# Optimization experiments

Hardware: AMD Instinct MI355X
Metric: run time of the kernel (lower is better)

Reference implementation:

```python
import jax, jax.numpy as jnp
import numpy as np

D_MODEL = 2048
N_HEADS = 16
HEAD_DIM = D_MODEL // N_HEADS


def _rotate_half(x):
    # matches torch: x1 = x[..., ::2], x2 = x[..., 1::2]; cat(-x2, x1)
    x1 = x[..., ::2]
    x2 = x[..., 1::2]
    return jnp.concatenate((-x2, x1), axis=-1)


def _rope_sin_cos(seq_len, dtype):
    # NOTE: module builds RoPE tables over the FULL d_model, then truncates to head_dim.
    inv_freq = 1.0 / (10000.0 ** (np.arange(0, D_MODEL, 2, dtype=np.float32) / D_MODEL))
    pos = np.arange(seq_len, dtype=np.float32)
    freqs = pos[:, None] * inv_freq[None, :]          # [S, d_model/2]
    sin = jnp.asarray(np.sin(freqs)[:, :HEAD_DIM], dtype=dtype)  # [S, head_dim]
    cos = jnp.asarray(np.cos(freqs)[:, :HEAD_DIM], dtype=dtype)
    return sin[None, None], cos[None, None]           # [1,1,S,head_dim]


def setup_inputs() -> dict:
    key = jax.random.key(0)
    ks = jax.random.split(key, 11)
    B, S = 2, 2048
    sc = 1.0 / np.sqrt(D_MODEL)
    inp = {
        "query": jax.random.normal(ks[0], (B, S, D_MODEL), jnp.float32),
        "key": jax.random.normal(ks[1], (B, S, D_MODEL), jnp.float32),
        "value": jax.random.normal(ks[2], (B, S, D_MODEL), jnp.float32),
        "Wq": jax.random.normal(ks[3], (D_MODEL, D_MODEL), jnp.float32) * sc,
        "bq": jnp.zeros((D_MODEL,), jnp.float32),
        "Wk": jax.random.normal(ks[4], (D_MODEL, D_MODEL), jnp.float32) * sc,
        "bk": jnp.zeros((D_MODEL,), jnp.float32),
        "Wv": jax.random.normal(ks[5], (D_MODEL, D_MODEL), jnp.float32) * sc,
        "bv": jnp.zeros((D_MODEL,), jnp.float32),
        "Wo": jax.random.normal(ks[6], (D_MODEL, D_MODEL), jnp.float32) * sc,
        "bo": jnp.zeros((D_MODEL,), jnp.float32),
    }
    return inp


def reference(query, key, value, Wq, bq, Wk, bk, Wv, bv, Wo, bo):
    B, S, _ = query.shape

    def split_heads(x):
        return x.reshape(B, S, N_HEADS, HEAD_DIM).transpose(0, 2, 1, 3)  # [B,H,S,d_k]

    Q = split_heads(query @ Wq.T + bq)
    K = split_heads(key @ Wk.T + bk)
    V = split_heads(value @ Wv.T + bv)

    sin, cos = _rope_sin_cos(S, Q.dtype)
    Q = Q * cos + _rotate_half(Q) * sin
    K = K * cos + _rotate_half(K) * sin

    scores = jnp.einsum("bhqd,bhkd->bhqk", Q, K) / np.sqrt(HEAD_DIM)
    probs = jax.nn.softmax(scores, axis=-1)  # dropout is identity at eval
    context = jnp.einsum("bhqk,bhkd->bhqd", probs, V)
    out = context.transpose(0, 2, 1, 3).reshape(B, S, D_MODEL)
    return out @ Wo.T + bo
```

## Files before the change

kernel.cpp:

```cpp
#include <hip/hip_runtime.h>
#include <hip/hip_bf16.h>

#define D_MODEL 2048
#define SEQ     2048
#define BATCH   2
#define NH      16
#define HD      128
#define MROWS   (BATCH*SEQ)

typedef __attribute__((ext_vector_type(8)))  short bf16x8;
typedef __attribute__((ext_vector_type(4)))  float f32x4;
typedef __attribute__((ext_vector_type(16))) float f32x16;
typedef __attribute__((ext_vector_type(4)))  unsigned int u32x4;

static __device__ __forceinline__ void lds16(const void* g, void* l) {
    __builtin_amdgcn_global_load_lds(
        (const __attribute__((address_space(1))) void*)g,
        (__attribute__((address_space(3))) void*)l,
        16, 0, 0);
}

static __device__ __forceinline__ unsigned int pk2(float a, float b) {
    const unsigned int lo = __bfloat16_as_ushort(__float2bfloat16(a));
    const unsigned int hh = __bfloat16_as_ushort(__float2bfloat16(b));
    return lo | (hh << 16);
}
static __device__ __forceinline__ unsigned short bfu(float a) {
    return __bfloat16_as_ushort(__float2bfloat16(a));
}

__global__ __launch_bounds__(256) void cvt_all(
    const float* __restrict__ q,  const float* __restrict__ k,  const float* __restrict__ v,
    const float* __restrict__ wq, const float* __restrict__ wk, const float* __restrict__ wv,
    const float* __restrict__ wo,
    unsigned short* __restrict__ qb, unsigned short* __restrict__ kb, unsigned short* __restrict__ vb,
    unsigned short* __restrict__ wqb, unsigned short* __restrict__ wkb,
    unsigned short* __restrict__ wvb, unsigned short* __restrict__ wob)
{
    const int b = blockIdx.x;
    const float* src; unsigned short* dst; int idx;
    if (b < 24576) {
        const int s = b >> 13;
        idx = (b & 8191)*256 + threadIdx.x;
        src = (s==0) ? q : (s==1) ? k : v;
        dst = (s==0) ? qb : (s==1) ? kb : vb;
    } else {
        const int bb = b - 24576;
        const int s = bb >> 12;
        idx = (bb & 4095)*256 + threadIdx.x;
        src = (s==0) ? wq : (s==1) ? wk : (s==2) ? wv : wo;
        dst = (s==0) ? wqb : (s==1) ? wkb : (s==2) ? wvb : wob;
    }
    const float4 a = ((const float4*)src)[idx];
    ushort4 o;
    o.x = bfu(a.x); o.y = bfu(a.y); o.z = bfu(a.z); o.w = bfu(a.w);
    ((ushort4*)dst)[idx] = o;
}

__global__ __launch_bounds__(256) void rope_table(float* __restrict__ tab)
{
    const int i = blockIdx.x*256 + threadIdx.x;
    const int s = i >> 7, d = i & 127;
    const float invf = expf(-(float)d * (9.210340371976184f / 1024.0f));
    const float f = (float)s * invf;
    tab[(size_t)s*256 + d]       = cosf(f);
    tab[(size_t)s*256 + 128 + d] = sinf(f);
}

__global__ __launch_bounds__(256, 2) void gemm_qkv_fused(
    const __hip_bfloat16* __restrict__ Aq,
    const __hip_bfloat16* __restrict__ Ak,
    const __hip_bfloat16* __restrict__ Av,
    const __hip_bfloat16* __restrict__ Wq, const __hip_bfloat16* __restrict__ Wk,
    const __hip_bfloat16* __restrict__ Wv,
    const float* __restrict__ bq, const float* __restrict__ bk, const float* __restrict__ bv,
    const float* __restrict__ tab,
    __hip_bfloat16* __restrict__ Qp, __hip_bfloat16* __restrict__ Kp,
    __hip_bfloat16* __restrict__ Vt)
{
    __shared__ char smem[65536];
    __hip_bfloat16* As = (__hip_bfloat16*)smem;
    __hip_bfloat16* Bs = (__hip_bfloat16*)(smem + 32768);

    const int K    = D_MODEL;
    const int bm   = blockIdx.x / 48;
    const int bn   = blockIdx.x % 48;
    const int mat  = bn >> 4;
    const int hd   = bn & 15;
    const __hip_bfloat16* A  = (mat==0) ? Aq : (mat==1) ? Ak : Av;
    const __hip_bfloat16* W  = (mat==0) ? Wq : (mat==1) ? Wk : Wv;
    const float*          bi = (mat==0) ? bq : (mat==1) ? bk : bv;

    const int tid  = threadIdx.x;
    const int lane = tid & 63;
    const int w    = tid >> 6;
    const int wr   = (w >> 1) * 64;
    const int wc   = (w & 1) * 64;
    const int l15  = lane & 15, l4 = lane >> 4;

    const int srow = w*32 + (lane>>2);
    const __hip_bfloat16* ga = A + (size_t)(bm*128 + srow)*K + (lane&3)*8;
    const __hip_bfloat16* gb = W + (size_t)(hd*128 + srow)*K + (lane&3)*8;

#define GSTAGE(Q_, KT_) do {                                               \
        lds16(ga + (KT_),                &As[(Q_)*4096 + (w*32)*32]);      \
        lds16(ga + (KT_) + (size_t)16*K, &As[(Q_)*4096 + (w*32+16)*32]);   \
        lds16(gb + (KT_),                &Bs[(Q_)*4096 + (w*32)*32]);      \
        lds16(gb + (KT_) + (size_t)16*K, &Bs[(Q_)*4096 + (w*32+16)*32]);   \
    } while (0)

    f32x4 acc[4][4] = {};
    const int NT = K >> 5;

    GSTAGE(0, 0);
    GSTAGE(1, 32);
    asm volatile("s_waitcnt vmcnt(4)" ::: "memory");
    __builtin_amdgcn_s_barrier();

    for (int t = 0; t < NT; ++t) {
        const int q = t & 3;
        if (t + 2 < NT) GSTAGE((t+2)&3, (t+2)*32);
        bf16x8 af[4], bfr[4];
        #pragma unroll
        for (int i = 0; i < 4; i++) {
            af[i]  = *(const bf16x8*)&As[q*4096 + (wr + i*16 + l15)*32 + l4*8];
            bfr[i] = *(const bf16x8*)&Bs[q*4096 + (wc + i*16 + l15)*32 + l4*8];
        }
        __builtin_amdgcn_s_setprio(1);
        #pragma unroll
        for (int i = 0; i < 4; i++)
            #pragma unroll
            for (int j = 0; j < 4; j++)
                acc[i][j] = __builtin_amdgcn_mfma_f32_16x16x32_bf16(af[i], bfr[j], acc[i][j], 0, 0, 0);
        __builtin_amdgcn_s_setprio(0);
        if (t + 2 < NT) {
            asm volatile("s_waitcnt vmcnt(4)" ::: "memory");
            __builtin_amdgcn_s_barrier();
        } else if (t + 1 < NT) {
            asm volatile("s_waitcnt vmcnt(0)" ::: "memory");
            __builtin_amdgcn_s_barrier();
        }
    }
#undef GSTAGE

    __syncthreads();
    float* Ct = (float*)smem;

    #pragma unroll
    for (int i = 0; i < 4; i++) {
        #pragma unroll
        for (int j = 0; j < 4; j++) {
            const int col = wc + j*16 + l15;
            const float bvv = bi[hd*128 + col];
            #pragma unroll
            for (int r = 0; r < 4; r++) {
                const int row = wr + i*16 + l4*4 + r;
                Ct[row*128 + (col ^ (row & 31))] = acc[i][j][r] + bvv;
            }
        }
    }
    __syncthreads();

    const int grow0 = bm*128;
    const int bb    = grow0 >> 11;
    const int s0    = grow0 & (SEQ-1);

    if (mat < 2) {
        __hip_bfloat16* Out = (mat==0) ? Qp : Kp;
        #pragma unroll
        for (int p = 0; p < 16; p++) {
            const int rl = p*8 + (tid>>5);
            const int c4 = (tid&31)*4;
            const int kx = rl & 31;
            const float* tc = tab + (size_t)(s0 + rl)*256;
            float o[4];
            #pragma unroll
            for (int i2 = 0; i2 < 4; i2++) {
                const int d  = c4 + i2;
                const float x  = Ct[rl*128 + (d ^ kx)];
                const int   pd = (d < 64) ? (2*d + 1) : (2*d - 128);
                const float xp = Ct[rl*128 + (pd ^ kx)];
                const float cs = tc[d], sn = tc[128 + d];
                o[i2] = (d < 64) ? (x*cs - xp*sn) : (x*cs + xp*sn);
            }
            ushort4 pkd;
            pkd.x = bfu(o[0]); pkd.y = bfu(o[1]); pkd.z = bfu(o[2]); pkd.w = bfu(o[3]);
            *(ushort4*)(Out + (size_t)(grow0 + rl)*D_MODEL + hd*HD + c4) = pkd;
        }
    } else {
        unsigned short* vt = (unsigned short*)Vt;
        #pragma unroll
        for (int p = 0; p < 16; p++) {
            const int d  = p*8 + (tid>>5);
            const int s4 = (tid&31)*4;
            float o[4];
            #pragma unroll
            for (int i2 = 0; i2 < 4; i2++) {
                const int sr = s4 + i2;
                o[i2] = Ct[sr*128 + (d ^ (sr & 31))];
            }
            ushort4 pkd;
            pkd.x = bfu(o[0]); pkd.y = bfu(o[1]); pkd.z = bfu(o[2]); pkd.w = bfu(o[3]);
            *(ushort4*)(vt + ((size_t)(bb*16 + hd)*HD + d)*SEQ + s0 + s4) = pkd;
        }
    }
}

__global__ __launch_bounds__(256, 2) void gemm_bt_bias_f32(
    const __hip_bfloat16* __restrict__ A,
    const __hip_bfloat16* __restrict__ W,
    const float* __restrict__ bias,
    float* __restrict__ C,
    const int M, const int N, const int K)
{
    __shared__ __hip_bfloat16 As[4][128*32];
    __shared__ __hip_bfloat16 Bs[4][128*32];
    const int nb   = N >> 7;
    const int bm   = blockIdx.x / nb;
    const int bn   = blockIdx.x % nb;
    const int tid  = threadIdx.x;
    const int lane = tid & 63;
    const int w    = tid >> 6;
    const int wr   = (w >> 1) * 64;
    const int wc   = (w & 1) * 64;
    const int l15  = lane & 15, l4 = lane >> 4;

    const int srow = w*32 + (lane>>2);
    const __hip_bfloat16* ga = A + (size_t)(bm*128 + srow)*K + (lane&3)*8;
    const __hip_bfloat16* gb = W + (size_t)(bn*128 + srow)*K + (lane&3)*8;

#define GSTAGE(Q_, KT_) do {                                          \
        lds16(ga + (KT_),                &As[Q_][(w*32)*32]);         \
        lds16(ga + (KT_) + (size_t)16*K, &As[Q_][(w*32+16)*32]);      \
        lds16(gb + (KT_),                &Bs[Q_][(w*32)*32]);         \
        lds16(gb + (KT_) + (size_t)16*K, &Bs[Q_][(w*32+16)*32]);      \
    } while (0)

    f32x4 acc[4][4] = {};
    const int NT = K >> 5;

    GSTAGE(0, 0);
    GSTAGE(1, 32);
    asm volatile("s_waitcnt vmcnt(4)" ::: "memory");
    __builtin_amdgcn_s_barrier();

    for (int t = 0; t < NT; ++t) {
        const int q = t & 3;
        if (t + 2 < NT) GSTAGE((t+2)&3, (t+2)*32);
        bf16x8 af[4], bfr[4];
        #pragma unroll
        for (int i = 0; i < 4; i++) {
            af[i]  = *(const bf16x8*)&As[q][(wr + i*16 + l15)*32 + l4*8];
            bfr[i] = *(const bf16x8*)&Bs[q][(wc + i*16 + l15)*32 + l4*8];
        }
        __builtin_amdgcn_s_setprio(1);
        #pragma unroll
        for (int i = 0; i < 4; i++)
            #pragma unroll
            for (int j = 0; j < 4; j++)
                acc[i][j] = __builtin_amdgcn_mfma_f32_16x16x32_bf16(af[i], bfr[j], acc[i][j], 0, 0, 0);
        __builtin_amdgcn_s_setprio(0);
        if (t + 2 < NT) {
            asm volatile("s_waitcnt vmcnt(4)" ::: "memory");
            __builtin_amdgcn_s_barrier();
        } else if (t + 1 < NT) {
            asm volatile("s_waitcnt vmcnt(0)" ::: "memory");
            __builtin_amdgcn_s_barrier();
        }
    }
#undef GSTAGE

    float bv[4];
    #pragma unroll
    for (int j = 0; j < 4; j++)
        bv[j] = bias[bn*128 + wc + j*16 + l15];
    #pragma unroll
    for (int i = 0; i < 4; i++) {
        #pragma unroll
        for (int j = 0; j < 4; j++) {
            const int col = bn*128 + wc + j*16 + l15;
            #pragma unroll
            for (int r = 0; r < 4; r++) {
                const int row = bm*128 + wr + i*16 + l4*4 + r;
                C[(size_t)row*N + col] = acc[i][j][r] + bv[j];
            }
        }
    }
}

__global__ __launch_bounds__(256, 2) void flash_attn(
    const __hip_bfloat16* __restrict__ Qg,
    const __hip_bfloat16* __restrict__ Kg,
    const __hip_bfloat16* __restrict__ Vtg,
    __hip_bfloat16* __restrict__ ctx)
{
    __shared__ __hip_bfloat16 Ks[2][64*128];
    __shared__ __hip_bfloat16 Vs[2][128*64];

    const int tid  = threadIdx.x;
    const int w    = tid >> 6;
    const int lane = tid & 63;
    const int l31  = lane & 31;
    const int hi   = lane >> 5;
    const bool hib = (hi != 0);

    const int bid0 = blockIdx.x;
    const int bid  = (bid0 & 7)*64 + (bid0 >> 3);
    const int bh   = bid >> 4;
    const int qt   = bid & 15;
    const int bi   = bh >> 4, h = bh & 15;
    const int q0   = qt * 128;

    const float SC = 0.08838834764831845f;

    bf16x8 aq[8];
    {
        const __hip_bfloat16* qp =
            Qg + (size_t)(bi*SEQ + q0 + w*32 + l31)*D_MODEL + h*HD + hi*8;
        #pragma unroll
        for (int ds = 0; ds < 8; ds++) aq[ds] = *(const bf16x8*)(qp + ds*16);
    }

#define STAGE(NB, KV) do {                                                              \
        _Pragma("unroll")                                                               \
        for (int i_ = 0; i_ < 4; i_++) {                                                \
            const int kr_ = w*16 + i_*4 + (lane>>4);                                    \
            lds16(Kg + (size_t)(bi*SEQ + (KV) + kr_)*D_MODEL + h*HD                     \
                      + (((lane&15) ^ (kr_&15))*8),                                     \
                  &Ks[NB][(w*16 + i_*4)*128]);                                          \
        }                                                                               \
        _Pragma("unroll")                                                               \
        for (int i_ = 0; i_ < 4; i_++) {                                                \
            const int vr_ = w*32 + i_*8 + (lane>>3);                                    \
            lds16(Vtg + ((size_t)bh*HD + vr_)*SEQ + (KV)                                \
                      + (((lane&7) ^ (lane>>3))*8),                                     \
                  &Vs[NB][(w*32 + i_*8)*64]);                                           \
        }                                                                               \
    } while (0)

    f32x16 o0 = {}, o1 = {}, o2 = {}, o3 = {};
    float m_run = -1e30f, l_run = 0.0f;

    STAGE(0, 0);

    for (int t = 0; t < SEQ/64; t++) {
        const int cb = t & 1;
        __syncthreads();
        if (t < SEQ/64 - 1) STAGE(cb^1, (t+1)*64);

        f32x16 p0 = {}, p1 = {};
        #pragma unroll
        for (int ds = 0; ds < 8; ds++) {
            const int sl = ((ds*2 + hi) ^ (lane&15)) * 8;
            const bf16x8 k0 = *(const bf16x8*)&Ks[cb][l31*128 + sl];
            const bf16x8 k1 = *(const bf16x8*)&Ks[cb][(32 + l31)*128 + sl];
            p0 = __builtin_amdgcn_mfma_f32_32x32x16_bf16(k0, aq[ds], p0, 0, 0, 0);
            p1 = __builtin_amdgcn_mfma_f32_32x32x16_bf16(k1, aq[ds], p1, 0, 0, 0);
        }

        float pm = fmaxf(p0[0], p1[0]);
        #pragma unroll
        for (int r = 1; r < 16; r++) pm = fmaxf(pm, fmaxf(p0[r], p1[r]));
        pm = fmaxf(pm, __shfl_xor(pm, 32));

        if (!__all(pm <= m_run + 90.509667f)) {
            const float mnew = fmaxf(m_run, pm);
            const float al = __expf((m_run - mnew) * SC);
            l_run *= al;
            m_run = mnew;
            float alr[16];
            #pragma unroll
            for (int r = 0; r < 16; r++)
                alr[r] = __shfl(al, (r&3) + 8*(r>>2) + (hib ? 4 : 0));
            #pragma unroll
            for (int r = 0; r < 16; r++) {
                o0[r] *= alr[r]; o1[r] *= alr[r]; o2[r] *= alr[r]; o3[r] *= alr[r];
            }
        }

        #pragma unroll
        for (int r = 0; r < 16; r++) {
            p0[r] = __expf((p0[r] - m_run) * SC);
            p1[r] = __expf((p1[r] - m_run) * SC);
        }
        float rs = 0.0f;
        #pragma unroll
        for (int r = 0; r < 16; r++) rs += p0[r] + p1[r];
        rs += __shfl_xor(rs, 32);
        l_run += rs;

#define PV_STEP(PF, KS) do {                                                            \
            const unsigned int A0_ = pk2(PF[8*((KS)&1)+0], PF[8*((KS)&1)+1]);           \
            const unsigned int A1_ = pk2(PF[8*((KS)&1)+2], PF[8*((KS)&1)+3]);           \
            const unsigned int B0_ = pk2(PF[8*((KS)&1)+4], PF[8*((KS)&1)+5]);           \
            const unsigned int B1_ = pk2(PF[8*((KS)&1)+6], PF[8*((KS)&1)+7]);           \
            const unsigned int s0_ = hib ? A0_ : B0_;                                   \
            const unsigned int s1_ = hib ? A1_ : B1_;                                   \
            const unsigned int r0_ = (unsigned int)__shfl_xor((int)s0_, 32);            \
            const unsigned int r1_ = (unsigned int)__shfl_xor((int)s1_, 32);            \
            u32x4 au_;                                                                  \
            au_.x = hib ? r0_ : A0_;  au_.y = hib ? r1_ : A1_;                          \
            au_.z = hib ? B0_ : r0_;  au_.w = hib ? B1_ : r1_;                          \
            const bf16x8 pa_ = *(const bf16x8*)&au_;                                    \
            const int ko_ = (((KS)*2 + hi) ^ (lane&7)) * 8;                             \
            o0 = __builtin_amdgcn_mfma_f32_32x32x16_bf16(pa_,                           \
                     *(const bf16x8*)&Vs[cb][(  0 + l31)*64 + ko_], o0, 0, 0, 0);       \
            o1 = __builtin_amdgcn_mfma_f32_32x32x16_bf16(pa_,                           \
                     *(const bf16x8*)&Vs[cb][( 32 + l31)*64 + ko_], o1, 0, 0, 0);       \
            o2 = __builtin_amdgcn_mfma_f32_32x32x16_bf16(pa_,                           \
                     *(const bf16x8*)&Vs[cb][( 64 + l31)*64 + ko_], o2, 0, 0, 0);       \
            o3 = __builtin_amdgcn_mfma_f32_32x32x16_bf16(pa_,                           \
                     *(const bf16x8*)&Vs[cb][( 96 + l31)*64 + ko_], o3, 0, 0, 0);       \
        } while (0)

        PV_STEP(p0, 0); PV_STEP(p0, 1); PV_STEP(p1, 2); PV_STEP(p1, 3);
#undef PV_STEP
    }

    const float inv = 1.0f / l_run;
    float invr[16];
    #pragma unroll
    for (int r = 0; r < 16; r++)
        invr[r] = __shfl(inv, (r&3) + 8*(r>>2) + (hib ? 4 : 0));

    #pragma unroll
    for (int r = 0; r < 16; r++) {
        const int qr = q0 + w*32 + (r&3) + 8*(r>>2) + (hib ? 4 : 0);
        __hip_bfloat16* cp = ctx + (size_t)(bi*SEQ + qr)*D_MODEL + h*HD + l31;
        cp[0]  = __float2bfloat16(o0[r] * invr[r]);
        cp[32] = __float2bfloat16(o1[r] * invr[r]);
        cp[64] = __float2bfloat16(o2[r] * invr[r]);
        cp[96] = __float2bfloat16(o3[r] * invr[r]);
    }
#undef STAGE
}

extern "C" void kernel_launch(void* const* d_in, const int* in_sizes, int n_in,
                              void* d_out, int out_size, void* d_ws, size_t ws_size,
                              hipStream_t stream)
{
    const float* query = (const float*)d_in[0];
    const float* key   = (const float*)d_in[1];
    const float* value = (const float*)d_in[2];
    const float* Wq    = (const float*)d_in[3];
    const float* bq    = (const float*)d_in[4];
    const float* Wk    = (const float*)d_in[5];
    const float* bk    = (const float*)d_in[6];
    const float* Wv    = (const float*)d_in[7];
    const float* bv    = (const float*)d_in[8];
    const float* Wo    = (const float*)d_in[9];
    const float* bo    = (const float*)d_in[10];
    float* out = (float*)d_out;

    char* ws = (char*)d_ws;
    const size_t MB = 1024*1024;
    __hip_bfloat16* qb  = (__hip_bfloat16*)(ws);
    __hip_bfloat16* kbuf= (__hip_bfloat16*)(ws + 16*MB);
    __hip_bfloat16* vbuf= (__hip_bfloat16*)(ws + 32*MB);
    __hip_bfloat16* Qp  = (__hip_bfloat16*)(ws + 48*MB);
    __hip_bfloat16* Kp  = (__hip_bfloat16*)(ws + 64*MB);
    __hip_bfloat16* Vt  = (__hip_bfloat16*)(ws + 80*MB);
    __hip_bfloat16* ctx = (__hip_bfloat16*)(ws + 96*MB);
    __hip_bfloat16* Wqb = (__hip_bfloat16*)(ws + 112*MB);
    __hip_bfloat16* Wkb = (__hip_bfloat16*)(ws + 120*MB);
    __hip_bfloat16* Wvb = (__hip_bfloat16*)(ws + 128*MB);
    __hip_bfloat16* Wob = (__hip_bfloat16*)(ws + 136*MB);
    float*          tab = (float*)         (ws + 144*MB);

    cvt_all<<<40960, 256, 0, stream>>>(query, key, value, Wq, Wk, Wv, Wo,
        (unsigned short*)qb, (unsigned short*)kbuf, (unsigned short*)vbuf,
        (unsigned short*)Wqb, (unsigned short*)Wkb, (unsigned short*)Wvb,
        (unsigned short*)Wob);

    rope_table<<<SEQ*HD/256, 256, 0, stream>>>(tab);

    gemm_qkv_fused<<<(MROWS/128)*48, 256, 0, stream>>>(
        qb, kbuf, vbuf, Wqb, Wkb, Wvb, bq, bk, bv, tab, Qp, Kp, Vt);

    flash_attn<<<BATCH*NH*(SEQ/128), 256, 0, stream>>>(Qp, Kp, Vt, ctx);

    gemm_bt_bias_f32<<<(MROWS/128)*(D_MODEL/128), 256, 0, stream>>>(
        ctx, Wob, bo, out, MROWS, D_MODEL, D_MODEL);
}
```

Before: 330.7 us.

## Drop LDS staging in flash attention, read K/V directly; swizzle GEMM block order

The flash attention kernel no longer stages K and V tiles through double-buffered shared memory with barriers. Each wave now loads its MFMA operands straight from global memory (relying on L2/L1 cache) and raises wave priority around the MFMA sections, and the launch-bounds occupancy hint is removed. Both GEMM kernels also remap block indices so groups of four row tiles share a column tile, which should improve L2 reuse. Direct global loads drop the LDS traffic and synchronisation but expose global latency inside the MFMA loop, with no prefetching and many redundant reads across waves. The GEMM remap hardcodes the grid shape.

```diff
diff --git a/kernel.cpp b/kernel.cpp
--- a/kernel.cpp
+++ b/kernel.cpp
@@ -83,8 +83,10 @@
     __hip_bfloat16* Bs = (__hip_bfloat16*)(smem + 32768);
 
     const int K    = D_MODEL;
-    const int bm   = blockIdx.x / 48;
-    const int bn   = blockIdx.x % 48;
+    const int x    = blockIdx.x & 7;
+    const int r    = blockIdx.x >> 3;
+    const int bn   = r >> 2;
+    const int bm   = x*4 + (r & 3);
     const int mat  = bn >> 4;
     const int hd   = bn & 15;
     const __hip_bfloat16* A  = (mat==0) ? Aq : (mat==1) ? Ak : Av;
@@ -153,9 +155,9 @@
             const int col = wc + j*16 + l15;
             const float bvv = bi[hd*128 + col];
             #pragma unroll
-            for (int r = 0; r < 4; r++) {
-                const int row = wr + i*16 + l4*4 + r;
-                Ct[row*128 + (col ^ (row & 31))] = acc[i][j][r] + bvv;
+            for (int rr = 0; rr < 4; rr++) {
+                const int row = wr + i*16 + l4*4 + rr;
+                Ct[row*128 + (col ^ (row & 31))] = acc[i][j][rr] + bvv;
             }
         }
     }
@@ -177,11 +179,11 @@
             #pragma unroll
             for (int i2 = 0; i2 < 4; i2++) {
                 const int d  = c4 + i2;
-                const float x  = Ct[rl*128 + (d ^ kx)];
+                const float xx = Ct[rl*128 + (d ^ kx)];
                 const int   pd = (d < 64) ? (2*d + 1) : (2*d - 128);
                 const float xp = Ct[rl*128 + (pd ^ kx)];
                 const float cs = tc[d], sn = tc[128 + d];
-                o[i2] = (d < 64) ? (x*cs - xp*sn) : (x*cs + xp*sn);
+                o[i2] = (d < 64) ? (xx*cs - xp*sn) : (xx*cs + xp*sn);
             }
             ushort4 pkd;
             pkd.x = bfu(o[0]); pkd.y = bfu(o[1]); pkd.z = bfu(o[2]); pkd.w = bfu(o[3]);
@@ -215,9 +217,10 @@
 {
     __shared__ __hip_bfloat16 As[4][128*32];
     __shared__ __hip_bfloat16 Bs[4][128*32];
-    const int nb   = N >> 7;
-    const int bm   = blockIdx.x / nb;
-    const int bn   = blockIdx.x % nb;
+    const int x    = blockIdx.x & 7;
+    const int r    = blockIdx.x >> 3;
+    const int bn   = r >> 2;
+    const int bm   = x*4 + (r & 3);
     const int tid  = threadIdx.x;
     const int lane = tid & 63;
     const int w    = tid >> 6;
@@ -280,23 +283,20 @@
         for (int j = 0; j < 4; j++) {
             const int col = bn*128 + wc + j*16 + l15;
             #pragma unroll
-            for (int r = 0; r < 4; r++) {
-                const int row = bm*128 + wr + i*16 + l4*4 + r;
-                C[(size_t)row*N + col] = acc[i][j][r] + bv[j];
+            for (int rr = 0; rr < 4; rr++) {
+                const int row = bm*128 + wr + i*16 + l4*4 + rr;
+                C[(size_t)row*N + col] = acc[i][j][rr] + bv[j];
             }
         }
     }
 }
 
-__global__ __launch_bounds__(256, 2) void flash_attn(
+__global__ __launch_bounds__(256) void flash_attn(
     const __hip_bfloat16* __restrict__ Qg,
     const __hip_bfloat16* __restrict__ Kg,
     const __hip_bfloat16* __restrict__ Vtg,
     __hip_bfloat16* __restrict__ ctx)
 {
-    __shared__ __hip_bfloat16 Ks[2][64*128];
-    __shared__ __hip_bfloat16 Vs[2][128*64];
-
     const int tid  = threadIdx.x;
     const int w    = tid >> 6;
     const int lane = tid & 63;
@@ -321,42 +321,26 @@
         for (int ds = 0; ds < 8; ds++) aq[ds] = *(const bf16x8*)(qp + ds*16);
     }
 
-#define STAGE(NB, KV) do {                                                              \
-        _Pragma("unroll")                                                               \
-        for (int i_ = 0; i_ < 4; i_++) {                                                \
-            const int kr_ = w*16 + i_*4 + (lane>>4);                                    \
-            lds16(Kg + (size_t)(bi*SEQ + (KV) + kr_)*D_MODEL + h*HD                     \
-                      + (((lane&15) ^ (kr_&15))*8),                                     \
-                  &Ks[NB][(w*16 + i_*4)*128]);                                          \
-        }                                                                               \
-        _Pragma("unroll")                                                               \
-        for (int i_ = 0; i_ < 4; i_++) {                                                \
-            const int vr_ = w*32 + i_*8 + (lane>>3);                                    \
-            lds16(Vtg + ((size_t)bh*HD + vr_)*SEQ + (KV)                                \
-                      + (((lane&7) ^ (lane>>3))*8),                                     \
-                  &Vs[NB][(w*32 + i_*8)*64]);                                           \
-        }                                                                               \
-    } while (0)
+    const __hip_bfloat16* kb = Kg  + (size_t)(bi*SEQ + l31)*D_MODEL + h*HD + hi*8;
+    const __hip_bfloat16* vb = Vtg + ((size_t)bh*HD + l31)*SEQ + hi*8;
 
     f32x16 o0 = {}, o1 = {}, o2 = {}, o3 = {};
     float m_run = -1e30f, l_run = 0.0f;
 
-    STAGE(0, 0);
-
     for (int t = 0; t < SEQ/64; t++) {
-        const int cb = t & 1;
-        __syncthreads();
-        if (t < SEQ/64 - 1) STAGE(cb^1, (t+1)*64);
+        const int kv = t*64;
+        const __hip_bfloat16* kc = kb + (size_t)kv*D_MODEL;
 
         f32x16 p0 = {}, p1 = {};
+        __builtin_amdgcn_s_setprio(1);
         #pragma unroll
         for (int ds = 0; ds < 8; ds++) {
-            const int sl = ((ds*2 + hi) ^ (lane&15)) * 8;
-            const bf16x8 k0 = *(const bf16x8*)&Ks[cb][l31*128 + sl];
-            const bf16x8 k1 = *(const bf16x8*)&Ks[cb][(32 + l31)*128 + sl];
+            const bf16x8 k0 = *(const bf16x8*)(kc + ds*16);
+            const bf16x8 k1 = *(const bf16x8*)(kc + (size_t)32*D_MODEL + ds*16);
             p0 = __builtin_amdgcn_mfma_f32_32x32x16_bf16(k0, aq[ds], p0, 0, 0, 0);
             p1 = __builtin_amdgcn_mfma_f32_32x32x16_bf16(k1, aq[ds], p1, 0, 0, 0);
         }
+        __builtin_amdgcn_s_setprio(0);
 
         float pm = fmaxf(p0[0], p1[0]);
         #pragma unroll
@@ -389,6 +373,7 @@
         rs += __shfl_xor(rs, 32);
         l_run += rs;
 
+        __builtin_amdgcn_s_setprio(1);
 #define PV_STEP(PF, KS) do {                                                            \
             const unsigned int A0_ = pk2(PF[8*((KS)&1)+0], PF[8*((KS)&1)+1]);           \
             const unsigned int A1_ = pk2(PF[8*((KS)&1)+2], PF[8*((KS)&1)+3]);           \
@@ -402,19 +387,20 @@
             au_.x = hib ? r0_ : A0_;  au_.y = hib ? r1_ : A1_;                          \
             au_.z = hib ? B0_ : r0_;  au_.w = hib ? B1_ : r1_;                          \
             const bf16x8 pa_ = *(const bf16x8*)&au_;                                    \
-            const int ko_ = (((KS)*2 + hi) ^ (lane&7)) * 8;                             \
+            const __hip_bfloat16* vp_ = vb + kv + (KS)*16;                              \
             o0 = __builtin_amdgcn_mfma_f32_32x32x16_bf16(pa_,                           \
-                     *(const bf16x8*)&Vs[cb][(  0 + l31)*64 + ko_], o0, 0, 0, 0);       \
+                     *(const bf16x8*)(vp_),                    o0, 0, 0, 0);            \
             o1 = __builtin_amdgcn_mfma_f32_32x32x16_bf16(pa_,                           \
-                     *(const bf16x8*)&Vs[cb][( 32 + l31)*64 + ko_], o1, 0, 0, 0);       \
+                     *(const bf16x8*)(vp_ + (size_t)32*SEQ),   o1, 0, 0, 0);            \
             o2 = __builtin_amdgcn_mfma_f32_32x32x16_bf16(pa_,                           \
-                     *(const bf16x8*)&Vs[cb][( 64 + l31)*64 + ko_], o2, 0, 0, 0);       \
+                     *(const bf16x8*)(vp_ + (size_t)64*SEQ),   o2, 0, 0, 0);            \
             o3 = __builtin_amdgcn_mfma_f32_32x32x16_bf16(pa_,                           \
-                     *(const bf16x8*)&Vs[cb][( 96 + l31)*64 + ko_], o3, 0, 0, 0);       \
+                     *(const bf16x8*)(vp_ + (size_t)96*SEQ),   o3, 0, 0, 0);            \
         } while (0)
 
         PV_STEP(p0, 0); PV_STEP(p0, 1); PV_STEP(p1, 2); PV_STEP(p1, 3);
 #undef PV_STEP
+        __builtin_amdgcn_s_setprio(0);
     }
 
     const float inv = 1.0f / l_run;
@@ -432,7 +418,6 @@
         cp[64] = __float2bfloat16(o2[r] * invr[r]);
         cp[96] = __float2bfloat16(o3[r] * invr[r]);
     }
-#undef STAGE
 }
 
 extern "C" void kernel_launch(void* const* d_in, const int* in_sizes, int n_in,
```

Result: slower. 503.0 us (+52.1%).
